# Kernel optimization log

Measured on AMD Instinct MI355X. Metric: run time of the kernel, lower is better.

Reference implementation:

```python
import math
import jax, jax.numpy as jnp
import numpy as np

# ---- SLAYER neuron / simulation constants (from config) ----
THETA = 10.0      # spike threshold
TAU_SR = 10.0     # PSP (SRM) kernel time constant
TAU_REF = 1.0     # refractory kernel time constant
TS = 1.0          # simulation time step
T_SAMPLE = 500    # number of time bins
B, N_IN, N_HID, N_OUT = 64, 1024, 1024, 10


def _alpha_kernel(tau, mult, eps=0.01):
    """slayer _calculateAlphaKernel: mult * t/tau * exp(1 - t/tau), truncated."""
    vals = []
    t = 0.0
    while t < T_SAMPLE:
        v = mult * t / tau * math.exp(1.0 - t / tau)
        if abs(v) < eps and t > tau:
            break
        vals.append(v)
        t += TS
    return np.asarray(vals, np.float32)

SRM_KERNEL = jnp.asarray(_alpha_kernel(TAU_SR, 1.0))            # [K]
REF_KERNEL = jnp.asarray(_alpha_kernel(TAU_REF, -2.0 * THETA))  # [Kr], REF_KERNEL[0] == 0


def dense(x, W):
    # per-timestep fully-connected layer (slayer.dense == 1x1x1 conv3d, no bias)
    # x: [B, Nin, T], W: [Nout, Nin] -> [B, Nout, T]
    return jnp.einsum('oi,bit->bot', W, x)


def psp(x):
    # causal temporal convolution with the SRM kernel: out[t] = Ts * sum_k srm[k] * x[t-k]
    Bx, N, T = x.shape
    K = SRM_KERNEL.shape[0]
    k = SRM_KERNEL[::-1].reshape(1, 1, K).astype(x.dtype)  # flip -> true convolution
    y = jax.lax.conv_general_dilated(
        x.reshape(Bx * N, 1, T), k, (1,), [(K - 1, 0)],
        dimension_numbers=('NCH', 'OIH', 'NCH'))
    return y.reshape(Bx, N, T) * TS


def spike_impl(u_in):
    # sequential LIF thresholding with refractory feedback (slayer spike kernel)
    # u_in: [B, N, T] membrane drive; returns (spikes, membrane) both [B, N, T]
    Kr = REF_KERNEL.shape[0]
    # buf[j] is the refractory contribution arriving at step t+j; new spike at t
    # contributes REF_KERNEL[j] at t+j (REF_KERNEL[0]==0), i.e. shifted kernel into buf.
    refk = jnp.concatenate([REF_KERNEL[1:], jnp.zeros((1,), u_in.dtype)]).astype(u_in.dtype)
    buf0 = jnp.zeros(u_in.shape[:-1] + (Kr,), u_in.dtype)

    def step(buf, u_t):
        u = u_t + buf[..., 0]                              # membrane at time t
        s = (u >= THETA).astype(u_in.dtype) / TS           # spike (amplitude 1/Ts)
        buf = jnp.concatenate([buf[..., 1:], jnp.zeros_like(buf[..., :1])], axis=-1)
        buf = buf + s[..., None] * refk
        return buf, (s, u)

    _, (s, u) = jax.lax.scan(step, buf0, jnp.moveaxis(u_in, -1, 0))
    return jnp.moveaxis(s, 0, -1), jnp.moveaxis(u, 0, -1)


def setup_inputs() -> dict:
    key = jax.random.key(0)
    k1, k2, k3 = jax.random.split(key, 3)
    spike_input = (jax.random.uniform(k1, (B, N_IN, T_SAMPLE)) < 0.05).astype(jnp.float32)
    W1 = jax.random.normal(k2, (N_HID, N_IN), jnp.float32) * 0.3
    W2 = jax.random.normal(k3, (N_OUT, N_HID), jnp.float32) * 0.3
    return {"spike_input": spike_input, "W1": W1, "W2": W2}


def reference(spike_input, W1, W2):
    s1, _ = spike_impl(psp(dense(spike_input, W1)))
    s2, _ = spike_impl(psp(dense(s1, W2)))
    return s2
```

## Files before the change

kernel.cpp:

```cpp
#include <hip/hip_runtime.h>
#include <stdint.h>
#include <math.h>

#define T_SIM 500
#define NB    64
#define NIN   1024
#define NHID  1024
#define NOUT  10
#define KSRM  77
#define CHUNK 32
#define TT    32
#define RING  108

__device__ __forceinline__ double srm_tap(int k) {
  double u = (double)k / 10.0;
  double v = u * exp(1.0 - u);
  return (double)(float)v;
}
__device__ __forceinline__ double ref_tap(int j) {
  double v = (-20.0 * (double)j) * exp(1.0 - (double)j);
  return (double)(float)v;
}

__global__ __launch_bounds__(64)
void k_pack(const float* __restrict__ x, unsigned long long* __restrict__ bits) {
  const int b = blockIdx.x, ig = blockIdx.y, tc = blockIdx.z;
  const int lane = threadIdx.x;
  const float* xr = x + ((size_t)b * NIN + ig * 64 + lane) * T_SIM;
  const int t0 = tc * 100;
  for (int t = t0; t < t0 + 100; t += 4) {
    const float4 v = *(const float4*)(xr + t);
    unsigned long long m0 = __ballot(v.x > 0.5f);
    unsigned long long m1 = __ballot(v.y > 0.5f);
    unsigned long long m2 = __ballot(v.z > 0.5f);
    unsigned long long m3 = __ballot(v.w > 0.5f);
    if (lane == 0) {
      unsigned long long* w = bits + (size_t)(b * T_SIM + t) * 16 + ig;
      w[0] = m0; w[16] = m1; w[32] = m2; w[48] = m3;
    }
  }
}

__global__ __launch_bounds__(256)
void k_transpose(const float* __restrict__ W1, float* __restrict__ W1T) {
  __shared__ float tile[64][65];
  const int bo = blockIdx.x * 64, bi = blockIdx.y * 64;
  for (int k = threadIdx.x; k < 4096; k += 256) {
    int r = k >> 6, c = k & 63;
    tile[r][c] = W1[(size_t)(bo + r) * NIN + bi + c];
  }
  __syncthreads();
  for (int k = threadIdx.x; k < 4096; k += 256) {
    int r = k >> 6, c = k & 63;
    W1T[(size_t)(bi + r) * NHID + bo + c] = tile[c][r];
  }
}

__global__ __launch_bounds__(128)
void k_dense1(const uint32_t* __restrict__ bits, const float* __restrict__ W1T,
              double* __restrict__ a1c, int col_base) {
  const int col_loc = blockIdx.x;
  const int half = blockIdx.y;
  const int o = half * 512 + threadIdx.x * 4;
  const uint32_t* w = bits + (size_t)(col_base + col_loc) * 32;
  double a0 = 0.0, a1 = 0.0, a2 = 0.0, a3 = 0.0;
  for (int wi = 0; wi < 32; ++wi) {
    uint32_t m = w[wi];
    const int ibase = wi * 32;
    while (m) {
      const int j = __ffs(m) - 1;
      m &= m - 1;
      const float4 wv = *(const float4*)(W1T + (size_t)(ibase + j) * NHID + o);
      a0 += (double)wv.x; a1 += (double)wv.y; a2 += (double)wv.z; a3 += (double)wv.w;
    }
  }
  double4 r; r.x = a0; r.y = a1; r.z = a2; r.w = a3;
  *(double4*)(a1c + (size_t)col_loc * NHID + o) = r;
}

__global__ __launch_bounds__(256)
void k_ps1(const double* __restrict__ a1c, unsigned long long* __restrict__ s1bits,
           int b_base) {
  __shared__ double S[RING * 64];
  __shared__ double Y[TT * 64];
  __shared__ double srm[KSRM];
  const int ng = blockIdx.x, b_loc = blockIdx.y;
  const int tid = threadIdx.x;
  if (tid < KSRM) srm[tid] = srm_tap(tid);
  for (int i = tid; i < RING * 64; i += 256) S[i] = 0.0;

  double refk[11];
#pragma unroll
  for (int j = 1; j <= 10; ++j) refk[j] = ref_tap(j);
  uint32_t smask = 0;

  const double* abase = a1c + (size_t)b_loc * T_SIM * NHID + ng * 64;
  unsigned long long* sbase =
      s1bits + (size_t)(b_base + b_loc) * T_SIM * 16 + ng;

  __syncthreads();

  for (int t0 = 0; t0 < T_SIM; t0 += TT) {
    const int tv = (T_SIM - t0 < TT) ? (T_SIM - t0) : TT;
    for (int e = tid; e < tv * 64; e += 256) {
      const int r = e >> 6, n = e & 63;
      const int t = t0 + r;
      S[(t % RING) * 64 + n] = abase[(size_t)t * NHID + n];
    }
    __syncthreads();
    {
      const int n = tid & 63, tq = tid >> 6;
      const int tl0 = tq * 8;
      double acc[8];
#pragma unroll
      for (int u = 0; u < 8; ++u) acc[u] = 0.0;
      int t = t0 + tl0 - 76;
      int m = t % RING; if (m < 0) m += RING;
#pragma unroll
      for (int s = 0; s < 84; ++s) {
        if (t >= 0) {
          const double v = S[m * 64 + n];
#pragma unroll
          for (int u = 0; u < 8; ++u) {
            const int k = 76 - s + u;
            if (k >= 0 && k < KSRM) acc[u] += srm[k] * v;
          }
        }
        ++t; ++m; if (m == RING) m = 0;
      }
#pragma unroll
      for (int u = 0; u < 8; ++u)
        if (tl0 + u < tv) Y[(tl0 + u) * 64 + n] = acc[u];
    }
    __syncthreads();
    if (tid < 64) {
      for (int g = 0; g < tv; ++g) {
        double u = Y[g * 64 + tid];
#pragma unroll
        for (int j = 10; j >= 1; --j)
          u += refk[j] * (double)((smask >> (j - 1)) & 1u);
        const bool sp = (u >= 10.0);
        smask = (smask << 1) | (sp ? 1u : 0u);
        const unsigned long long bm = __ballot(sp);
        if (tid == 0) sbase[(size_t)(t0 + g) * 16] = bm;
      }
    }
    __syncthreads();
  }
}

__global__ __launch_bounds__(256)
void k_dense2(const unsigned long long* __restrict__ s1bits,
              const float* __restrict__ W2, double* __restrict__ a2) {
  __shared__ float w2t[NHID * NOUT];
  for (int k = threadIdx.x; k < NHID * NOUT; k += 256) {
    const int o = k >> 10, i = k & 1023;
    w2t[i * NOUT + o] = W2[k];
  }
  __syncthreads();
  const int col = blockIdx.x * 256 + threadIdx.x;
  double acc[NOUT];
#pragma unroll
  for (int o = 0; o < NOUT; ++o) acc[o] = 0.0;
  const unsigned long long* w = s1bits + (size_t)col * 16;
  for (int wi = 0; wi < 16; ++wi) {
    unsigned long long m = w[wi];
    const int ibase = wi * 64;
    while (m) {
      const int j = __ffsll(m) - 1;
      m &= m - 1;
      const float* row = &w2t[(ibase + j) * NOUT];
#pragma unroll
      for (int o = 0; o < NOUT; ++o) acc[o] += (double)row[o];
    }
  }
  double* outp = a2 + (size_t)col * NOUT;
#pragma unroll
  for (int o = 0; o < NOUT; ++o) outp[o] = acc[o];
}

__global__ __launch_bounds__(256)
void k_l2(const double* __restrict__ a2, float* __restrict__ out) {
  __shared__ double S[T_SIM * NOUT];
  __shared__ double Y[T_SIM * NOUT];
  __shared__ double srm[KSRM];
  const int b = blockIdx.x, tid = threadIdx.x;
  if (tid < KSRM) srm[tid] = srm_tap(tid);
  for (int i = tid; i < T_SIM * NOUT; i += 256)
    S[i] = a2[(size_t)b * T_SIM * NOUT + i];
  __syncthreads();
  for (int i = tid; i < T_SIM * NOUT; i += 256) {
    const int t = i / 10, o = i - t * 10;
    const int kmax = (t < KSRM - 1) ? t : (KSRM - 1);
    double acc = 0.0;
    for (int k = 0; k <= kmax; ++k)
      acc += srm[k] * S[(t - k) * 10 + o];
    Y[i] = acc;
  }
  __syncthreads();
  if (tid < NOUT) {
    double refk[11];
#pragma unroll
    for (int j = 1; j <= 10; ++j) refk[j] = ref_tap(j);
    uint32_t smask = 0;
    float* op = out + ((size_t)b * NOUT + tid) * T_SIM;
    for (int t = 0; t < T_SIM; ++t) {
      double u = Y[t * 10 + tid];
#pragma unroll
      for (int j = 10; j >= 1; --j)
        u += refk[j] * (double)((smask >> (j - 1)) & 1u);
      const bool sp = (u >= 10.0);
      smask = (smask << 1) | (sp ? 1u : 0u);
      op[t] = sp ? 1.0f : 0.0f;
    }
  }
}

extern "C" void kernel_launch(void* const* d_in, const int* in_sizes, int n_in,
                              void* d_out, int out_size, void* d_ws, size_t ws_size,
                              hipStream_t stream) {
  const float* x  = (const float*)d_in[0];
  const float* W1 = (const float*)d_in[1];
  const float* W2 = (const float*)d_in[2];
  float* out = (float*)d_out;

  char* ws = (char*)d_ws;
  unsigned long long* bits1 = (unsigned long long*)(ws);
  float*  W1T = (float*) (ws + 4096000);
  double* a1c = (double*)(ws + 8290304);
  unsigned long long* s1bits = (unsigned long long*)(ws + 139362304);
  double* a2  = (double*)(ws + 143458304);

  hipLaunchKernelGGL(k_pack, dim3(NB, 16, 5), dim3(64), 0, stream, x, bits1);
  hipLaunchKernelGGL(k_transpose, dim3(16, 16), dim3(256), 0, stream, W1, W1T);

  for (int bc = 0; bc < NB; bc += CHUNK) {
    hipLaunchKernelGGL(k_dense1, dim3(CHUNK * T_SIM, 2), dim3(128), 0, stream,
                       (const uint32_t*)bits1, W1T, a1c, bc * T_SIM);
    hipLaunchKernelGGL(k_ps1, dim3(16, CHUNK), dim3(256), 0, stream,
                       a1c, s1bits, bc);
  }

  hipLaunchKernelGGL(k_dense2, dim3(125), dim3(256), 0, stream, s1bits, W2, a2);
  hipLaunchKernelGGL(k_l2, dim3(NB), dim3(256), 0, stream, a2, out);
}
```

Before: 1.054 ms.

## Compact active-input lists in dense1 and narrow PSP blocks with prefetch

k_dense1 now builds a shared-memory list of active input indices with a warp prefix sum. It then has 256 threads cover all 1024 outputs in one block, unrolling four independent rows per step, instead of each thread walking bitmasks with ffs. k_ps1 switches to 32-neuron groups, which doubles the block count. It also prefetches the next time chunk into registers while computing, and uses a sliding-tap convolution over a larger ring buffer to drop the per-tap branches. Layer-1 spikes are stored as 32-bit words, and dense2 reads them that way. The costs are extra shared memory and a list-building phase that runs before any FMA work.

```diff
diff --git a/kernel.cpp b/kernel.cpp
--- a/kernel.cpp
+++ b/kernel.cpp
@@ -10,7 +10,7 @@
 #define KSRM  77
 #define CHUNK 32
 #define TT    32
-#define RING  108
+#define RING  140
 
 __device__ __forceinline__ double srm_tap(int k) {
   double u = (double)k / 10.0;
@@ -56,118 +56,189 @@
   }
 }
 
-__global__ __launch_bounds__(128)
+__global__ __launch_bounds__(256)
 void k_dense1(const uint32_t* __restrict__ bits, const float* __restrict__ W1T,
               double* __restrict__ a1c, int col_base) {
+  __shared__ int list[NIN];
+  __shared__ int nact_s;
   const int col_loc = blockIdx.x;
-  const int half = blockIdx.y;
-  const int o = half * 512 + threadIdx.x * 4;
-  const uint32_t* w = bits + (size_t)(col_base + col_loc) * 32;
-  double a0 = 0.0, a1 = 0.0, a2 = 0.0, a3 = 0.0;
+  const int tid = threadIdx.x;
+  if (tid < 32) {
+    uint32_t w = bits[(size_t)(col_base + col_loc) * 32 + tid];
+    int c = __popc(w);
+    int p = c;
+#pragma unroll
+    for (int d = 1; d < 32; d <<= 1) {
+      int q = __shfl_up(p, d);
+      if (tid >= d) p += q;
+    }
+    int excl = p - c;
+    while (w) {
+      const int j = __ffs(w) - 1;
+      w &= w - 1;
+      list[excl++] = tid * 32 + j;
+    }
+    if (tid == 31) nact_s = excl;
+  }
+  __syncthreads();
+  const int n = nact_s;
+  const int o = tid * 4;
+  double a0x=0,a0y=0,a0z=0,a0w=0, a1x=0,a1y=0,a1z=0,a1w=0;
+  double a2x=0,a2y=0,a2z=0,a2w=0, a3x=0,a3y=0,a3z=0,a3w=0;
+  int g = 0;
+  for (; g + 4 <= n; g += 4) {
+    const int i0 = list[g], i1 = list[g+1], i2 = list[g+2], i3 = list[g+3];
+    const float4 w0 = *(const float4*)(W1T + (size_t)i0 * NHID + o);
+    const float4 w1 = *(const float4*)(W1T + (size_t)i1 * NHID + o);
+    const float4 w2 = *(const float4*)(W1T + (size_t)i2 * NHID + o);
+    const float4 w3 = *(const float4*)(W1T + (size_t)i3 * NHID + o);
+    a0x += (double)w0.x; a0y += (double)w0.y; a0z += (double)w0.z; a0w += (double)w0.w;
+    a1x += (double)w1.x; a1y += (double)w1.y; a1z += (double)w1.z; a1w += (double)w1.w;
+    a2x += (double)w2.x; a2y += (double)w2.y; a2z += (double)w2.z; a2w += (double)w2.w;
+    a3x += (double)w3.x; a3y += (double)w3.y; a3z += (double)w3.z; a3w += (double)w3.w;
+  }
+  if (g + 0 < n) {
+    const float4 wv = *(const float4*)(W1T + (size_t)list[g+0] * NHID + o);
+    a0x += (double)wv.x; a0y += (double)wv.y; a0z += (double)wv.z; a0w += (double)wv.w;
+  }
+  if (g + 1 < n) {
+    const float4 wv = *(const float4*)(W1T + (size_t)list[g+1] * NHID + o);
+    a1x += (double)wv.x; a1y += (double)wv.y; a1z += (double)wv.z; a1w += (double)wv.w;
+  }
+  if (g + 2 < n) {
+    const float4 wv = *(const float4*)(W1T + (size_t)list[g+2] * NHID + o);
+    a2x += (double)wv.x; a2y += (double)wv.y; a2z += (double)wv.z; a2w += (double)wv.w;
+  }
+  double4 r;
+  r.x = (a0x + a1x) + (a2x + a3x);
+  r.y = (a0y + a1y) + (a2y + a3y);
+  r.z = (a0z + a1z) + (a2z + a3z);
+  r.w = (a0w + a1w) + (a2w + a3w);
+  *(double4*)(a1c + (size_t)col_loc * NHID + o) = r;
+}
+
+__global__ __launch_bounds__(256)
+void k_ps1(const double* __restrict__ a1c, uint32_t* __restrict__ s1w,
+           int b_base) {
+  __shared__ double S[RING * 32];
+  __shared__ double Y[TT * 32];
+  __shared__ double srm[KSRM];
+  const int ng = blockIdx.x, b_loc = blockIdx.y;
+  const int tid = threadIdx.x;
+  if (tid < KSRM) srm[tid] = srm_tap(tid);
+
+  double refk[11];
+#pragma unroll
+  for (int j = 1; j <= 10; ++j) refk[j] = ref_tap(j);
+  uint32_t smask = 0;
+
+  const double* __restrict__ abase = a1c + (size_t)b_loc * T_SIM * NHID + ng * 32;
+  uint32_t* __restrict__ sbase =
+      s1w + (size_t)(b_base + b_loc) * T_SIM * 32 + ng;
+
+  double pf[4];
+  {
+#pragma unroll
+    for (int j = 0; j < 4; ++j) {
+      const int id = tid + j * 256;
+      const int r = id >> 5, n = id & 31;
+      pf[j] = abase[(size_t)r * NHID + n];
+    }
+    for (int i = tid; i < RING * 32; i += 256) S[i] = 0.0;
+    __syncthreads();
+#pragma unroll
+    for (int j = 0; j < 4; ++j) {
+      const int id = tid + j * 256;
+      const int r = id >> 5, n = id & 31;
+      S[((r) % RING) * 32 + n] = pf[j];
+    }
+    __syncthreads();
+  }
+
+  for (int t0 = 0; t0 < T_SIM; t0 += TT) {
+    const int tv = (T_SIM - t0 < TT) ? (T_SIM - t0) : TT;
+    const int t0n = t0 + TT;
+    const int tvn = (t0n >= T_SIM) ? 0 : ((T_SIM - t0n < TT) ? (T_SIM - t0n) : TT);
+#pragma unroll
+    for (int j = 0; j < 4; ++j) {
+      const int id = tid + j * 256;
+      if (id < tvn * 32) {
+        const int r = id >> 5, n = id & 31;
+        pf[j] = abase[(size_t)(t0n + r) * NHID + n];
+      }
+    }
+    {
+      const int n = tid & 31, tq = tid >> 5;
+      const int tbase = t0 + tq * 4 - 76;
+      int m0 = tbase % RING; if (m0 < 0) m0 += RING;
+      int len1 = RING - m0; if (len1 > 80) len1 = 80;
+      double tap0 = 0.0, tap1 = 0.0, tap2 = 0.0, tap3 = 0.0;
+      double c0 = 0.0, c1 = 0.0, c2 = 0.0, c3 = 0.0;
+      int s = 0;
+#pragma unroll 4
+      for (; s < len1; ++s) {
+        const double v = S[(m0 + s) * 32 + n];
+        tap3 = tap2; tap2 = tap1; tap1 = tap0;
+        tap0 = (s <= 76) ? srm[76 - s] : 0.0;
+        c0 += tap0 * v; c1 += tap1 * v; c2 += tap2 * v; c3 += tap3 * v;
+      }
+#pragma unroll 4
+      for (; s < 80; ++s) {
+        const double v = S[(s - len1) * 32 + n];
+        tap3 = tap2; tap2 = tap1; tap1 = tap0;
+        tap0 = (s <= 76) ? srm[76 - s] : 0.0;
+        c0 += tap0 * v; c1 += tap1 * v; c2 += tap2 * v; c3 += tap3 * v;
+      }
+      const int tl = tq * 4;
+      if (tl + 0 < tv) Y[(tl + 0) * 32 + n] = c0;
+      if (tl + 1 < tv) Y[(tl + 1) * 32 + n] = c1;
+      if (tl + 2 < tv) Y[(tl + 2) * 32 + n] = c2;
+      if (tl + 3 < tv) Y[(tl + 3) * 32 + n] = c3;
+    }
+    __syncthreads();
+    if (tid < 32) {
+      for (int g = 0; g < tv; ++g) {
+        double u = Y[g * 32 + tid];
+#pragma unroll
+        for (int j = 10; j >= 1; --j)
+          u += refk[j] * (double)((smask >> (j - 1)) & 1u);
+        const bool sp = (u >= 10.0);
+        smask = (smask << 1) | (sp ? 1u : 0u);
+        const unsigned long long bm = __ballot(sp);
+        if (tid == 0) sbase[(size_t)(t0 + g) * 32] = (uint32_t)bm;
+      }
+    }
+#pragma unroll
+    for (int j = 0; j < 4; ++j) {
+      const int id = tid + j * 256;
+      if (id < tvn * 32) {
+        const int r = id >> 5, n = id & 31;
+        S[((t0n + r) % RING) * 32 + n] = pf[j];
+      }
+    }
+    __syncthreads();
+  }
+}
+
+__global__ __launch_bounds__(256)
+void k_dense2(const uint32_t* __restrict__ s1w,
+              const float* __restrict__ W2, double* __restrict__ a2) {
+  __shared__ float w2t[NHID * NOUT];
+  for (int k = threadIdx.x; k < NHID * NOUT; k += 256) {
+    const int o = k >> 10, i = k & 1023;
+    w2t[i * NOUT + o] = W2[k];
+  }
+  __syncthreads();
+  const int col = blockIdx.x * 256 + threadIdx.x;
+  double acc[NOUT];
+#pragma unroll
+  for (int o = 0; o < NOUT; ++o) acc[o] = 0.0;
+  const uint32_t* w = s1w + (size_t)col * 32;
   for (int wi = 0; wi < 32; ++wi) {
     uint32_t m = w[wi];
     const int ibase = wi * 32;
     while (m) {
       const int j = __ffs(m) - 1;
-      m &= m - 1;
-      const float4 wv = *(const float4*)(W1T + (size_t)(ibase + j) * NHID + o);
-      a0 += (double)wv.x; a1 += (double)wv.y; a2 += (double)wv.z; a3 += (double)wv.w;
-    }
-  }
-  double4 r; r.x = a0; r.y = a1; r.z = a2; r.w = a3;
-  *(double4*)(a1c + (size_t)col_loc * NHID + o) = r;
-}
-
-__global__ __launch_bounds__(256)
-void k_ps1(const double* __restrict__ a1c, unsigned long long* __restrict__ s1bits,
-           int b_base) {
-  __shared__ double S[RING * 64];
-  __shared__ double Y[TT * 64];
-  __shared__ double srm[KSRM];
-  const int ng = blockIdx.x, b_loc = blockIdx.y;
-  const int tid = threadIdx.x;
-  if (tid < KSRM) srm[tid] = srm_tap(tid);
-  for (int i = tid; i < RING * 64; i += 256) S[i] = 0.0;
-
-  double refk[11];
-#pragma unroll
-  for (int j = 1; j <= 10; ++j) refk[j] = ref_tap(j);
-  uint32_t smask = 0;
-
-  const double* abase = a1c + (size_t)b_loc * T_SIM * NHID + ng * 64;
-  unsigned long long* sbase =
-      s1bits + (size_t)(b_base + b_loc) * T_SIM * 16 + ng;
-
-  __syncthreads();
-
-  for (int t0 = 0; t0 < T_SIM; t0 += TT) {
-    const int tv = (T_SIM - t0 < TT) ? (T_SIM - t0) : TT;
-    for (int e = tid; e < tv * 64; e += 256) {
-      const int r = e >> 6, n = e & 63;
-      const int t = t0 + r;
-      S[(t % RING) * 64 + n] = abase[(size_t)t * NHID + n];
-    }
-    __syncthreads();
-    {
-      const int n = tid & 63, tq = tid >> 6;
-      const int tl0 = tq * 8;
-      double acc[8];
-#pragma unroll
-      for (int u = 0; u < 8; ++u) acc[u] = 0.0;
-      int t = t0 + tl0 - 76;
-      int m = t % RING; if (m < 0) m += RING;
-#pragma unroll
-      for (int s = 0; s < 84; ++s) {
-        if (t >= 0) {
-          const double v = S[m * 64 + n];
-#pragma unroll
-          for (int u = 0; u < 8; ++u) {
-            const int k = 76 - s + u;
-            if (k >= 0 && k < KSRM) acc[u] += srm[k] * v;
-          }
-        }
-        ++t; ++m; if (m == RING) m = 0;
-      }
-#pragma unroll
-      for (int u = 0; u < 8; ++u)
-        if (tl0 + u < tv) Y[(tl0 + u) * 64 + n] = acc[u];
-    }
-    __syncthreads();
-    if (tid < 64) {
-      for (int g = 0; g < tv; ++g) {
-        double u = Y[g * 64 + tid];
-#pragma unroll
-        for (int j = 10; j >= 1; --j)
-          u += refk[j] * (double)((smask >> (j - 1)) & 1u);
-        const bool sp = (u >= 10.0);
-        smask = (smask << 1) | (sp ? 1u : 0u);
-        const unsigned long long bm = __ballot(sp);
-        if (tid == 0) sbase[(size_t)(t0 + g) * 16] = bm;
-      }
-    }
-    __syncthreads();
-  }
-}
-
-__global__ __launch_bounds__(256)
-void k_dense2(const unsigned long long* __restrict__ s1bits,
-              const float* __restrict__ W2, double* __restrict__ a2) {
-  __shared__ float w2t[NHID * NOUT];
-  for (int k = threadIdx.x; k < NHID * NOUT; k += 256) {
-    const int o = k >> 10, i = k & 1023;
-    w2t[i * NOUT + o] = W2[k];
-  }
-  __syncthreads();
-  const int col = blockIdx.x * 256 + threadIdx.x;
-  double acc[NOUT];
-#pragma unroll
-  for (int o = 0; o < NOUT; ++o) acc[o] = 0.0;
-  const unsigned long long* w = s1bits + (size_t)col * 16;
-  for (int wi = 0; wi < 16; ++wi) {
-    unsigned long long m = w[wi];
-    const int ibase = wi * 64;
-    while (m) {
-      const int j = __ffsll(m) - 1;
       m &= m - 1;
       const float* row = &w2t[(ibase + j) * NOUT];
 #pragma unroll
@@ -228,19 +299,19 @@
   unsigned long long* bits1 = (unsigned long long*)(ws);
   float*  W1T = (float*) (ws + 4096000);
   double* a1c = (double*)(ws + 8290304);
-  unsigned long long* s1bits = (unsigned long long*)(ws + 139362304);
+  uint32_t* s1w = (uint32_t*)(ws + 139362304);
   double* a2  = (double*)(ws + 143458304);
 
   hipLaunchKernelGGL(k_pack, dim3(NB, 16, 5), dim3(64), 0, stream, x, bits1);
   hipLaunchKernelGGL(k_transpose, dim3(16, 16), dim3(256), 0, stream, W1, W1T);
 
   for (int bc = 0; bc < NB; bc += CHUNK) {
-    hipLaunchKernelGGL(k_dense1, dim3(CHUNK * T_SIM, 2), dim3(128), 0, stream,
+    hipLaunchKernelGGL(k_dense1, dim3(CHUNK * T_SIM), dim3(256), 0, stream,
                        (const uint32_t*)bits1, W1T, a1c, bc * T_SIM);
-    hipLaunchKernelGGL(k_ps1, dim3(16, CHUNK), dim3(256), 0, stream,
-                       a1c, s1bits, bc);
-  }
-
-  hipLaunchKernelGGL(k_dense2, dim3(125), dim3(256), 0, stream, s1bits, W2, a2);
+    hipLaunchKernelGGL(k_ps1, dim3(32, CHUNK), dim3(256), 0, stream,
+                       a1c, s1w, bc);
+  }
+
+  hipLaunchKernelGGL(k_dense2, dim3(125), dim3(256), 0, stream, s1w, W2, a2);
   hipLaunchKernelGGL(k_l2, dim3(NB), dim3(256), 0, stream, a2, out);
 }
```

Result: slower. 1.093 ms (+3.7%).
